# Kernel tuning notes

Measured on AMD Instinct MI355X. Metric: run time of the kernel, lower is better.

Reference implementation:

```python
import jax, jax.numpy as jnp
import numpy as np

KERNEL_MUL = 10.0
KERNEL_NUM = 5


def _multi_kernel(dist, n_samples):
    # bandwidth estimated from detached distances (torch uses .data)
    bw = jax.lax.stop_gradient(jnp.sum(dist)) / (n_samples * n_samples - n_samples)
    bw = bw / (KERNEL_MUL ** (KERNEL_NUM // 2))
    k = jnp.zeros_like(dist)
    for i in range(KERNEL_NUM):
        k = k + jnp.exp(-dist / (bw * KERNEL_MUL ** i))
    return k


def setup_inputs() -> dict:
    key = jax.random.key(0)
    k1, k2 = jax.random.split(key)
    B, D = 256, 512
    source = jax.random.normal(k1, (B, D), dtype=jnp.float32)
    target = jax.random.normal(k2, (B, D), dtype=jnp.float32)
    return {"source": source, "target": target}


def reference(source, target):
    B = source.shape[0]
    src = source.reshape(B, -1)
    tgt = target.reshape(target.shape[0], -1)
    total = jnp.concatenate([src, tgt], axis=0)  # [N, D], N = 2B
    N = total.shape[0]

    # L2 pairwise distances via norm expansion (avoids [N,N,D] intermediate)
    sq = jnp.sum(total * total, axis=1)  # [N]
    L2 = jnp.maximum(sq[:, None] + sq[None, :] - 2.0 * (total @ total.T), 0.0)

    # L1 pairwise distances (structurally needs pairwise diffs)
    L1 = jnp.sum(jnp.abs(total[:, None, :] - total[None, :, :]), axis=-1)  # [N, N]

    kernels = _multi_kernel(L2, N) + _multi_kernel(L1, N)

    XX = kernels[:B, :B]
    YY = kernels[B:, B:]
    XY = kernels[:B, B:]
    YX = kernels[B:, :B]
    return jnp.mean(XX + YY - XY - YX)
```

## Files before the change

kernel.cpp:

```cpp
#include <hip/hip_runtime.h>

#define NROWS 512
#define BHALF 256
#define DIM   512
#define TILE  64
#define DCHUNK 128
#define NCHUNK 4
#define NN (NROWS * NROWS)


#define ACC(A, Bb, IV, JV)                                    \
    {                                                         \
        const float d_ = (IV) - (JV);                         \
        a2[A][Bb] = fmaf(d_, d_, a2[A][Bb]);                  \
        a1[A][Bb] += fabsf(d_);                               \
    }

#define STEP(DD)                                              \
    {                                                         \
        const float4 ivv = *(const float4*)&ai[DD][ty4];      \
        const float4 jvv = *(const float4*)&aj[DD][tx4];      \
        ACC(0, 0, ivv.x, jvv.x) ACC(0, 1, ivv.x, jvv.y)       \
        ACC(0, 2, ivv.x, jvv.z) ACC(0, 3, ivv.x, jvv.w)       \
        ACC(1, 0, ivv.y, jvv.x) ACC(1, 1, ivv.y, jvv.y)       \
        ACC(1, 2, ivv.y, jvv.z) ACC(1, 3, ivv.y, jvv.w)       \
        ACC(2, 0, ivv.z, jvv.x) ACC(2, 1, ivv.z, jvv.y)       \
        ACC(2, 2, ivv.z, jvv.z) ACC(2, 3, ivv.z, jvv.w)       \
        ACC(3, 0, ivv.w, jvv.x) ACC(3, 1, ivv.w, jvv.y)       \
        ACC(3, 2, ivv.w, jvv.z) ACC(3, 3, ivv.w, jvv.w)       \
    }

__global__ __launch_bounds__(256) void k_dist(const float* __restrict__ src,
                                              const float* __restrict__ tgt,
                                              float* __restrict__ ws)
{
    __shared__ float ai[DCHUNK][TILE];
    __shared__ float aj[DCHUNK][TILE];

    const int tj = blockIdx.x;
    const int ti = blockIdx.y;
    const int dc = blockIdx.z;
    const int t  = threadIdx.x;

    {
        const int r  = t & 63;
        const int dg = t >> 6;
        const int gi = ti * TILE + r;
        const int gj = tj * TILE + r;
        const float* prow_i = (gi < BHALF ? src + (size_t)gi * DIM
                                          : tgt + (size_t)(gi - BHALF) * DIM) + dc * DCHUNK;
        const float* prow_j = (gj < BHALF ? src + (size_t)gj * DIM
                                          : tgt + (size_t)(gj - BHALF) * DIM) + dc * DCHUNK;
#pragma unroll
        for (int k = 0; k < 8; ++k) {
            const int d4 = dg * 8 + k;
            const float4 vi = *(const float4*)(prow_i + d4 * 4);
            const float4 vj = *(const float4*)(prow_j + d4 * 4);
            ai[d4 * 4 + 0][r] = vi.x; ai[d4 * 4 + 1][r] = vi.y;
            ai[d4 * 4 + 2][r] = vi.z; ai[d4 * 4 + 3][r] = vi.w;
            aj[d4 * 4 + 0][r] = vj.x; aj[d4 * 4 + 1][r] = vj.y;
            aj[d4 * 4 + 2][r] = vj.z; aj[d4 * 4 + 3][r] = vj.w;
        }
    }
    __syncthreads();

    const int tx  = t & 15;
    const int ty  = t >> 4;
    const int tx4 = tx * 4;
    const int ty4 = ty * 4;

    float a2[4][4], a1[4][4];
#pragma unroll
    for (int a = 0; a < 4; ++a)
#pragma unroll
        for (int b = 0; b < 4; ++b) { a2[a][b] = 0.f; a1[a][b] = 0.f; }

#pragma unroll 2
    for (int d = 0; d < DCHUNK; d += 2) {
        STEP(d)
        STEP(d + 1)
    }

    float* part2 = ws + (size_t)dc * NN;
    float* part1 = ws + (size_t)(NCHUNK + dc) * NN;
    const int gj0 = tj * TILE + tx4;
#pragma unroll
    for (int a = 0; a < 4; ++a) {
        const int gi = ti * TILE + ty4 + a;
        const float4 s2 = make_float4(a2[a][0], a2[a][1], a2[a][2], a2[a][3]);
        const float4 s1 = make_float4(a1[a][0], a1[a][1], a1[a][2], a1[a][3]);
        *(float4*)&part2[(size_t)gi * NROWS + gj0] = s2;
        *(float4*)&part1[(size_t)gi * NROWS + gj0] = s1;
    }

    float s2 = 0.f, s1 = 0.f;
#pragma unroll
    for (int a = 0; a < 4; ++a)
#pragma unroll
        for (int b = 0; b < 4; ++b) { s2 += a2[a][b]; s1 += a1[a][b]; }
#pragma unroll
    for (int off = 32; off > 0; off >>= 1) {
        s2 += __shfl_down(s2, off);
        s1 += __shfl_down(s1, off);
    }
    __syncthreads();
    float* red = &ai[0][0];
    const int wave = t >> 6;
    if ((t & 63) == 0) { red[wave * 2] = s2; red[wave * 2 + 1] = s1; }
    __syncthreads();
    if (t == 0) {
        const float t2 = red[0] + red[2] + red[4] + red[6];
        const float t1 = red[1] + red[3] + red[5] + red[7];
        atomicAdd(ws + 8 * NN, t2);
        atomicAdd(ws + 8 * NN + 1, t1);
    }
}

__global__ __launch_bounds__(256) void k_mmd(const float* __restrict__ ws,
                                             float* __restrict__ out)
{
    const float S2 = ws[8 * NN];
    const float S1 = ws[8 * NN + 1];
    const float r2 = 26163200.0f / S2;
    const float r1 = 26163200.0f / S1;

    float acc = 0.f;
    const int base = blockIdx.x * 1024 + threadIdx.x;
#pragma unroll
    for (int q = 0; q < 4; ++q) {
        const int idx = base + q * 256;
        const float l2 = ws[idx] + ws[NN + idx] + ws[2 * NN + idx] + ws[3 * NN + idx];
        const float l1 = ws[4 * NN + idx] + ws[5 * NN + idx] + ws[6 * NN + idx] + ws[7 * NN + idx];
        float kv = 0.f;
        float f2 = r2, f1 = r1;
#pragma unroll
        for (int tt = 0; tt < 5; ++tt) {
            kv += __expf(-l2 * f2) + __expf(-l1 * f1);
            f2 *= 0.1f;
            f1 *= 0.1f;
        }
        const int i = idx >> 9;
        const int j = idx & 511;
        const float sgn = (((i ^ j) & BHALF) == 0) ? 1.0f : -1.0f;
        acc += sgn * kv;
    }
#pragma unroll
    for (int off = 32; off > 0; off >>= 1) acc += __shfl_down(acc, off);

    __shared__ float red[4];
    if ((threadIdx.x & 63) == 0) red[threadIdx.x >> 6] = acc;
    __syncthreads();
    if (threadIdx.x == 0) {
        const float s = red[0] + red[1] + red[2] + red[3];
        atomicAdd(out, s * (1.0f / 65536.0f));
    }
}

extern "C" void kernel_launch(void* const* d_in, const int* in_sizes, int n_in,
                              void* d_out, int out_size, void* d_ws, size_t ws_size,
                              hipStream_t stream)
{
    const float* src = (const float*)d_in[0];
    const float* tgt = (const float*)d_in[1];
    float* ws  = (float*)d_ws;
    float* out = (float*)d_out;

    hipMemsetAsync(ws + 8 * NN, 0, 2 * sizeof(float), stream);
    hipMemsetAsync(out, 0, sizeof(float), stream);

    dim3 g1(8, 8, 4);
    k_dist<<<g1, 256, 0, stream>>>(src, tgt, ws);
    k_mmd<<<256, 256, 0, stream>>>(ws, out);
}
```

Measured before the change: 84.74 us.

## Split distance reduction into more D-chunks and replace bandwidth atomics with partial sums

Halves the D-chunk size and doubles the chunk count, so the distance kernel launches 512 blocks instead of 256 and fills more compute units. The global atomic accumulation of the bandwidth sums, and the memset that cleared it, are replaced by per-block partial sums that every mmd block reduces itself. The cost is twice as much partial-distance workspace written and then read back in the second kernel, plus one extra memset-free reduction step per mmd block.

```diff
diff --git a/kernel.cpp b/kernel.cpp
--- a/kernel.cpp
+++ b/kernel.cpp
@@ -4,9 +4,10 @@
 #define BHALF 256
 #define DIM   512
 #define TILE  64
-#define DCHUNK 128
-#define NCHUNK 4
+#define DCHUNK 64
+#define NCHUNK 8
 #define NN (NROWS * NROWS)
+#define SOFF (16 * NN)
 
 
 #define ACC(A, Bb, IV, JV)                                    \
@@ -52,8 +53,8 @@
         const float* prow_j = (gj < BHALF ? src + (size_t)gj * DIM
                                           : tgt + (size_t)(gj - BHALF) * DIM) + dc * DCHUNK;
 #pragma unroll
-        for (int k = 0; k < 8; ++k) {
-            const int d4 = dg * 8 + k;
+        for (int k = 0; k < 4; ++k) {
+            const int d4 = dg * 4 + k;
             const float4 vi = *(const float4*)(prow_i + d4 * 4);
             const float4 vj = *(const float4*)(prow_j + d4 * 4);
             ai[d4 * 4 + 0][r] = vi.x; ai[d4 * 4 + 1][r] = vi.y;
@@ -75,7 +76,7 @@
 #pragma unroll
         for (int b = 0; b < 4; ++b) { a2[a][b] = 0.f; a1[a][b] = 0.f; }
 
-#pragma unroll 2
+#pragma unroll 4
     for (int d = 0; d < DCHUNK; d += 2) {
         STEP(d)
         STEP(d + 1)
@@ -109,28 +110,43 @@
     if ((t & 63) == 0) { red[wave * 2] = s2; red[wave * 2 + 1] = s1; }
     __syncthreads();
     if (t == 0) {
-        const float t2 = red[0] + red[2] + red[4] + red[6];
-        const float t1 = red[1] + red[3] + red[5] + red[7];
-        atomicAdd(ws + 8 * NN, t2);
-        atomicAdd(ws + 8 * NN + 1, t1);
+        const int bid = (dc * 8 + ti) * 8 + tj;
+        ws[SOFF + bid]       = red[0] + red[2] + red[4] + red[6];
+        ws[SOFF + 512 + bid] = red[1] + red[3] + red[5] + red[7];
     }
 }
 
 __global__ __launch_bounds__(256) void k_mmd(const float* __restrict__ ws,
                                              float* __restrict__ out)
 {
-    const float S2 = ws[8 * NN];
-    const float S1 = ws[8 * NN + 1];
+    const int t = threadIdx.x;
+    __shared__ float sred[8];
+
+    float sp2 = ws[SOFF + t] + ws[SOFF + 256 + t];
+    float sp1 = ws[SOFF + 512 + t] + ws[SOFF + 768 + t];
+#pragma unroll
+    for (int off = 32; off > 0; off >>= 1) {
+        sp2 += __shfl_down(sp2, off);
+        sp1 += __shfl_down(sp1, off);
+    }
+    if ((t & 63) == 0) { sred[(t >> 6) * 2] = sp2; sred[(t >> 6) * 2 + 1] = sp1; }
+    __syncthreads();
+    const float S2 = sred[0] + sred[2] + sred[4] + sred[6];
+    const float S1 = sred[1] + sred[3] + sred[5] + sred[7];
     const float r2 = 26163200.0f / S2;
     const float r1 = 26163200.0f / S1;
 
     float acc = 0.f;
-    const int base = blockIdx.x * 1024 + threadIdx.x;
+    const int base = blockIdx.x * 1024 + t;
 #pragma unroll
     for (int q = 0; q < 4; ++q) {
         const int idx = base + q * 256;
-        const float l2 = ws[idx] + ws[NN + idx] + ws[2 * NN + idx] + ws[3 * NN + idx];
-        const float l1 = ws[4 * NN + idx] + ws[5 * NN + idx] + ws[6 * NN + idx] + ws[7 * NN + idx];
+        float l2 = 0.f, l1 = 0.f;
+#pragma unroll
+        for (int c = 0; c < NCHUNK; ++c) {
+            l2 += ws[(size_t)c * NN + idx];
+            l1 += ws[(size_t)(NCHUNK + c) * NN + idx];
+        }
         float kv = 0.f;
         float f2 = r2, f1 = r1;
 #pragma unroll
@@ -147,11 +163,11 @@
 #pragma unroll
     for (int off = 32; off > 0; off >>= 1) acc += __shfl_down(acc, off);
 
-    __shared__ float red[4];
-    if ((threadIdx.x & 63) == 0) red[threadIdx.x >> 6] = acc;
     __syncthreads();
-    if (threadIdx.x == 0) {
-        const float s = red[0] + red[1] + red[2] + red[3];
+    if ((t & 63) == 0) sred[t >> 6] = acc;
+    __syncthreads();
+    if (t == 0) {
+        const float s = sred[0] + sred[1] + sred[2] + sred[3];
         atomicAdd(out, s * (1.0f / 65536.0f));
     }
 }
@@ -165,10 +181,9 @@
     float* ws  = (float*)d_ws;
     float* out = (float*)d_out;
 
-    hipMemsetAsync(ws + 8 * NN, 0, 2 * sizeof(float), stream);
     hipMemsetAsync(out, 0, sizeof(float), stream);
 
-    dim3 g1(8, 8, 4);
+    dim3 g1(8, 8, 8);
     k_dist<<<g1, 256, 0, stream>>>(src, tgt, ws);
     k_mmd<<<256, 256, 0, stream>>>(ws, out);
 }
```

After: 83.23 us. About the same (-1.8%).
